# Performance work log

Hardware: AMD Instinct MI355X
Metric: run time of the kernel (lower is better)

Reference implementation:

```python
import jax, jax.numpy as jnp
import numpy as np

B, S, D, H, F = 2, 2048, 2048, 16, 8192
HD = D // H  # 128
EPS = 1e-5


def setup_inputs() -> dict:
    key = jax.random.key(0)
    ks = jax.random.split(key, 10)
    s = 0.02
    return {
        "x": jax.random.normal(ks[0], (B, S, D), dtype=jnp.float32),
        "rms_w": jnp.ones((D,), dtype=jnp.float32),
        "w_qkv": jax.random.normal(ks[1], (3 * D, D), dtype=jnp.float32) * s,
        "w_out": jax.random.normal(ks[2], (D, D), dtype=jnp.float32) * s,
        "w1": jax.random.normal(ks[3], (F, D), dtype=jnp.float32) * s,
        "b1": jnp.zeros((F,), dtype=jnp.float32),
        "w3": jax.random.normal(ks[4], (F, D), dtype=jnp.float32) * s,
        "b3": jnp.zeros((F,), dtype=jnp.float32),
        "w2": jax.random.normal(ks[5], (D, F), dtype=jnp.float32) * s,
        "b2": jnp.zeros((D,), dtype=jnp.float32),
    }


def reference(x, rms_w, w_qkv, w_out, w1, b1, w3, b3, w2, b2):
    b, s, d = x.shape
    # RMSNorm (computed in fp32 as in original)
    xf = x.astype(jnp.float32)
    xn = (xf * jax.lax.rsqrt(jnp.mean(xf * xf, axis=-1, keepdims=True) + EPS)).astype(x.dtype) * rms_w
    # QKV projection: Linear(dim, 3*dim, bias=False) then 'b n (qkv h d) -> qkv b h n d'
    qkv = jnp.einsum('bsd,ed->bse', xn, w_qkv).reshape(b, s, 3, H, HD)
    qkv = jnp.transpose(qkv, (2, 0, 3, 1, 4))  # [3, b, h, s, hd]
    q, k, v = qkv[0], qkv[1], qkv[2]
    # Naive causal attention with explicit [b,h,s,s] score matrix
    scores = jnp.einsum('bhqd,bhkd->bhqk', q, k) / jnp.sqrt(jnp.float32(HD)).astype(x.dtype)
    causal = jnp.tril(jnp.ones((s, s), dtype=bool))
    scores = jnp.where(causal[None, None], scores, -jnp.inf)
    p = jax.nn.softmax(scores, axis=-1)
    # dropout p=0.0 -> identity
    out = jnp.einsum('bhqk,bhkd->bhqd', p, v)
    # Faithful to original: .view(bs, seqlen, h*d) on [b,h,s,hd] = raw row-major reshape
    out = out.reshape(b, s, H * HD)
    h = out @ w_out.T
    # FeedForward: w2(w1(h) + relu(w3(h))), biases per nn.Linear defaults
    ffn = ((h @ w1.T + b1) + jax.nn.relu(h @ w3.T + b3)) @ w2.T + b2
    return x + ffn
```

## Files before the change

kernel.cpp:

```cpp
#include <hip/hip_runtime.h>
#include <hip/hip_bf16.h>
#include <cstdint>

#define BB 2
#define SS 2048
#define DD 2048
#define HH 16
#define HD 128
#define FF 8192
#define QKVD 6144

typedef __bf16 bf16x8 __attribute__((ext_vector_type(8)));
typedef float floatx4 __attribute__((ext_vector_type(4)));

#define LOG2E 1.4426950408889634f

__device__ __forceinline__ unsigned short f2bf(float f) {
  unsigned u = __builtin_bit_cast(unsigned, f);
  u += 0x7FFFu + ((u >> 16) & 1u);
  return (unsigned short)(u >> 16);
}
__device__ __forceinline__ float bf2f(unsigned short h) {
  return __builtin_bit_cast(float, (unsigned)h << 16);
}

__device__ __forceinline__ void load_lds_16B(const void* g, void* l) {
  __builtin_amdgcn_global_load_lds(
      (const __attribute__((address_space(1))) unsigned int*)g,
      (__attribute__((address_space(3))) unsigned int*)l, 16, 0, 0);
}

__global__ void f32_to_bf16_vec(const float* __restrict__ src,
                                unsigned short* __restrict__ dst, int n4) {
  int i = blockIdx.x * 256 + threadIdx.x;
  if (i < n4) {
    float4 v = ((const float4*)src)[i];
    ushort4 o;
    o.x = f2bf(v.x); o.y = f2bf(v.y); o.z = f2bf(v.z); o.w = f2bf(v.w);
    ((ushort4*)dst)[i] = o;
  }
}

__global__ __launch_bounds__(256) void rmsnorm_bf16(const float* __restrict__ x,
                                                    const float* __restrict__ w,
                                                    unsigned short* __restrict__ xn) {
  const int row = blockIdx.x, tid = threadIdx.x;
  const float4* xr = (const float4*)(x + (size_t)row * DD);
  float4 a = xr[tid], b = xr[tid + 256];
  float ss = a.x * a.x + a.y * a.y + a.z * a.z + a.w * a.w +
             b.x * b.x + b.y * b.y + b.z * b.z + b.w * b.w;
#pragma unroll
  for (int off = 1; off < 64; off <<= 1) ss += __shfl_xor(ss, off);
  __shared__ float red[4];
  if ((tid & 63) == 0) red[tid >> 6] = ss;
  __syncthreads();
  float tot = red[0] + red[1] + red[2] + red[3];
  float sc = rsqrtf(tot * (1.0f / (float)DD) + 1e-5f);
  const float4* wr = (const float4*)w;
  float4 wa = wr[tid], wb = wr[tid + 256];
  ushort4 oa, ob;
  oa.x = f2bf(a.x * sc * wa.x); oa.y = f2bf(a.y * sc * wa.y);
  oa.z = f2bf(a.z * sc * wa.z); oa.w = f2bf(a.w * sc * wa.w);
  ob.x = f2bf(b.x * sc * wb.x); ob.y = f2bf(b.y * sc * wb.y);
  ob.z = f2bf(b.z * sc * wb.z); ob.w = f2bf(b.w * sc * wb.w);
  *(ushort4*)&xn[(size_t)row * DD + tid * 4] = oa;
  *(ushort4*)&xn[(size_t)row * DD + (tid + 256) * 4] = ob;
}

template <int MODE>
__global__ __launch_bounds__(512, 1) void gemm_bt(
    const unsigned short* __restrict__ A, const unsigned short* __restrict__ Bw,
    void* __restrict__ Cout, const float* __restrict__ bias,
    const unsigned short* __restrict__ aux, const float* __restrict__ res,
    int M, int N, int K) {
  __shared__ __align__(16) unsigned short As[2][2][128 * 64];
  __shared__ __align__(16) unsigned short Bs[2][2][128 * 64];
  const int tid = threadIdx.x;
  const int lane = tid & 63, w = tid >> 6;
  const int l16 = lane & 15, quad = lane >> 4;
  const int wm = w >> 2, wn = w & 3;

  const int gx = gridDim.x;
  const int nwg = gx * gridDim.y;
  const int bid = blockIdx.y * gx + blockIdx.x;
  const int cpx = nwg >> 3;
  const int swzb = (bid & 7) * cpx + (bid >> 3);
  const int n0 = (swzb % gx) * 256, m0 = (swzb / gx) * 256;

  const int NT = K >> 6, NIT = NT >> 1;

  const int sr = lane >> 3, sc = lane & 7;
  const unsigned short* pA0 = A + (size_t)(m0 + w * 8 + sr) * K + (sc ^ sr) * 8;
  const unsigned short* pA1 = pA0 + (size_t)128 * K;
  const unsigned short* pB0 =
      Bw + (size_t)(n0 + (w >> 2) * 64 + (w & 3) * 8 + sr) * K + (sc ^ sr) * 8;
  const unsigned short* pB1 = pB0 + (size_t)128 * K;

#define STAGE_A(d, h, kt)                                              \
  {                                                                    \
    const int _k = ((kt) < NT ? (kt) : NT - 1) * 64;                   \
    const size_t _ho = (size_t)(h) * 64 * K;                           \
    load_lds_16B(pA0 + _ho + _k, &As[d][h][(w * 8) * 64]);             \
    load_lds_16B(pA1 + _ho + _k, &As[d][h][(64 + w * 8) * 64]);        \
  }
#define STAGE_B(d, h, kt)                                              \
  {                                                                    \
    const int _k = ((kt) < NT ? (kt) : NT - 1) * 64;                   \
    const size_t _ho = (size_t)(h) * 32 * K;                           \
    load_lds_16B(pB0 + _ho + _k, &Bs[d][h][(w * 8) * 64]);             \
    load_lds_16B(pB1 + _ho + _k, &Bs[d][h][(64 + w * 8) * 64]);        \
  }

  floatx4 acc[2][2][4][2];
#pragma unroll
  for (int a0 = 0; a0 < 2; a0++)
#pragma unroll
    for (int a1 = 0; a1 < 2; a1++)
#pragma unroll
      for (int a2 = 0; a2 < 4; a2++)
#pragma unroll
        for (int a3 = 0; a3 < 2; a3++) acc[a0][a1][a2][a3] = floatx4{0.f, 0.f, 0.f, 0.f};
  bf16x8 bb[2][2];

#define PHASE(d, mq, nq, LOADB, STAGES, VMW)                                    \
  {                                                                             \
    bf16x8 a_[4][2];                                                            \
    _Pragma("unroll") for (int fr = 0; fr < 4; ++fr) {                          \
      const int lr_ = wm * 64 + fr * 16 + l16;                                  \
      _Pragma("unroll") for (int kc = 0; kc < 2; ++kc)                          \
        a_[fr][kc] = *(const bf16x8*)&As[d][mq]                                 \
            [lr_ * 64 + (((kc * 4 + quad) ^ (l16 & 7)) * 8)];                   \
    }                                                                           \
    if (LOADB) {                                                                \
      _Pragma("unroll") for (int fn = 0; fn < 2; ++fn) {                        \
        const int lr_ = wn * 32 + fn * 16 + l16;                                \
        _Pragma("unroll") for (int kc = 0; kc < 2; ++kc)                        \
          bb[fn][kc] = *(const bf16x8*)&Bs[d][nq]                               \
              [lr_ * 64 + (((kc * 4 + quad) ^ (l16 & 7)) * 8)];                 \
      }                                                                         \
    }                                                                           \
    STAGES                                                                      \
    __builtin_amdgcn_s_barrier();                                               \
    asm volatile("s_waitcnt lgkmcnt(0)" ::: "memory");                          \
    __builtin_amdgcn_sched_barrier(0);                                          \
    __builtin_amdgcn_s_setprio(1);                                              \
    _Pragma("unroll") for (int kc = 0; kc < 2; ++kc)                            \
      _Pragma("unroll") for (int fr = 0; fr < 4; ++fr)                          \
        _Pragma("unroll") for (int fn = 0; fn < 2; ++fn)                        \
          acc[mq][nq][fr][fn] = __builtin_amdgcn_mfma_f32_16x16x32_bf16(        \
              a_[fr][kc], bb[fn][kc], acc[mq][nq][fr][fn], 0, 0, 0);            \
    __builtin_amdgcn_s_setprio(0);                                              \
    if (VMW) asm volatile("s_waitcnt vmcnt(4)" ::: "memory");                   \
    __builtin_amdgcn_s_barrier();                                               \
    asm volatile("" ::: "memory");                                              \
  }

  STAGE_A(0, 0, 0)
  STAGE_A(0, 1, 0)
  STAGE_B(0, 0, 0)
  STAGE_B(0, 1, 0)
  STAGE_B(1, 0, 1)
  STAGE_A(1, 0, 1)
  asm volatile("s_waitcnt vmcnt(4)" ::: "memory");
  __builtin_amdgcn_s_barrier();
  asm volatile("" ::: "memory");

#pragma unroll 1
  for (int it = 0; it < NIT; ++it) {
    const int t1 = 2 * it + 1, tn0 = 2 * it + 2, tn1 = 2 * it + 3;
    PHASE(0, 0, 0, true,  STAGE_A(1, 1, t1) STAGE_B(1, 1, t1), false)
    PHASE(0, 1, 0, false, , false)
    PHASE(0, 0, 1, true,  STAGE_B(0, 0, tn0), false)
    PHASE(0, 1, 1, false, STAGE_A(0, 0, tn0), true)
    PHASE(1, 0, 0, true,  STAGE_A(0, 1, tn0) STAGE_B(0, 1, tn0), false)
    PHASE(1, 1, 0, false, , false)
    PHASE(1, 0, 1, true,  STAGE_B(1, 0, tn1), false)
    PHASE(1, 1, 1, false, STAGE_A(1, 0, tn1), true)
  }
  asm volatile("s_waitcnt vmcnt(0)" ::: "memory");
#undef PHASE
#undef STAGE_A
#undef STAGE_B

#pragma unroll
  for (int nq = 0; nq < 2; ++nq)
#pragma unroll
    for (int fn = 0; fn < 2; ++fn) {
      const int col = n0 + wn * 64 + nq * 32 + fn * 16 + l16;
      float bv = 0.0f;
      if constexpr (MODE >= 1) bv = bias[col];
#pragma unroll
      for (int mq = 0; mq < 2; ++mq)
#pragma unroll
        for (int fr = 0; fr < 4; ++fr) {
          const int row0 = m0 + wm * 128 + mq * 64 + fr * 16 + quad * 4;
#pragma unroll
          for (int r = 0; r < 4; ++r) {
            const size_t idx = (size_t)(row0 + r) * N + col;
            float v = acc[mq][nq][fr][fn][r];
            if constexpr (MODE == 0) {
              ((unsigned short*)Cout)[idx] = f2bf(v);
            } else if constexpr (MODE == 1) {
              ((unsigned short*)Cout)[idx] = f2bf(v + bv);
            } else if constexpr (MODE == 2) {
              float t = fmaxf(v + bv, 0.0f) + bf2f(aux[idx]);
              ((unsigned short*)Cout)[idx] = f2bf(t);
            } else {
              ((float*)Cout)[idx] = v + bv + res[idx];
            }
          }
        }
    }
}

__global__ __launch_bounds__(256) void attn_fwd(const unsigned short* __restrict__ qkv,
                                                unsigned short* __restrict__ out) {
  __shared__ __align__(16) unsigned short Ks[64 * 136];
  __shared__ __align__(16) unsigned short Vt[128 * 72];
  __shared__ __align__(16) unsigned short Ps[4][32 * 72];
  const int tid = threadIdx.x;
  const int lane = tid & 63, wave = tid >> 6;
  const int l16 = lane & 15, quad = lane >> 4;
  const int p = blockIdx.x, h = blockIdx.y, b = blockIdx.z;
  const float scale = 0.088388347648318447f;

#pragma unroll 1
  for (int pass = 0; pass < 2; pass++) {
    const int qt = pass == 0 ? 15 - p : p;
    const int q0w = qt * 128 + wave * 32;
    const int ntiles = 2 * qt + 2;

    bf16x8 aq[2][4];
#pragma unroll
    for (int mi = 0; mi < 2; mi++) {
      const unsigned short* Qp =
          qkv + (size_t)(b * SS + q0w + mi * 16 + l16) * QKVD + h * HD + quad * 8;
#pragma unroll
      for (int kc = 0; kc < 4; kc++) aq[mi][kc] = *(const bf16x8*)(Qp + kc * 32);
    }

    floatx4 o[2][8];
    float m_r[2][4], l_r[2][4];
#pragma unroll
    for (int mi = 0; mi < 2; mi++) {
#pragma unroll
      for (int nb = 0; nb < 8; nb++) o[mi][nb] = floatx4{0.f, 0.f, 0.f, 0.f};
#pragma unroll
      for (int r = 0; r < 4; r++) { m_r[mi][r] = -1e30f; l_r[mi][r] = 0.f; }
    }

#pragma unroll 1
    for (int t = 0; t < ntiles; t++) {
      const int kv0 = t * 64;
      const bool need_mask = (t >= ntiles - 2);
      __syncthreads();
      {
        const int cc = tid & 15;
#pragma unroll
        for (int i = 0; i < 4; i++) {
          const int r = (tid >> 4) + 16 * i;
          const size_t rowb = (size_t)(b * SS + kv0 + r) * QKVD + h * HD + cc * 8;
          *(uint4*)&Ks[r * 136 + cc * 8] = *(const uint4*)(qkv + rowb + DD);
          unsigned short tmp[8];
          *(uint4*)tmp = *(const uint4*)(qkv + rowb + 2 * DD);
#pragma unroll
          for (int j2 = 0; j2 < 8; j2++) {
            const int d = cc * 8 + j2;
            Vt[d * 72 + (((r >> 3) + (d >> 3)) & 7) * 8 + (r & 7)] = tmp[j2];
          }
        }
      }
      __syncthreads();

      floatx4 s[2][4];
#pragma unroll
      for (int mi = 0; mi < 2; mi++)
#pragma unroll
        for (int ni = 0; ni < 4; ni++) s[mi][ni] = floatx4{0.f, 0.f, 0.f, 0.f};
#pragma unroll
      for (int kc = 0; kc < 4; kc++) {
        bf16x8 bk[4];
#pragma unroll
        for (int ni = 0; ni < 4; ni++)
          bk[ni] = *(const bf16x8*)&Ks[(ni * 16 + l16) * 136 + kc * 32 + quad * 8];
#pragma unroll
        for (int mi = 0; mi < 2; mi++)
#pragma unroll
          for (int ni = 0; ni < 4; ni++)
            s[mi][ni] = __builtin_amdgcn_mfma_f32_16x16x32_bf16(aq[mi][kc], bk[ni],
                                                                s[mi][ni], 0, 0, 0);
      }

#pragma unroll
      for (int mi = 0; mi < 2; mi++) {
        float alpha[4];
#pragma unroll
        for (int r = 0; r < 4; r++) {
          const int qrow = q0w + mi * 16 + quad * 4 + r;
          float v[4];
#pragma unroll
          for (int ni = 0; ni < 4; ni++) {
            v[ni] = s[mi][ni][r] * scale;
            if (need_mask && (kv0 + ni * 16 + l16 > qrow)) v[ni] = -1e30f;
          }
          float mx = fmaxf(fmaxf(v[0], v[1]), fmaxf(v[2], v[3]));
          mx = fmaxf(mx, __shfl_xor(mx, 1));
          mx = fmaxf(mx, __shfl_xor(mx, 2));
          mx = fmaxf(mx, __shfl_xor(mx, 4));
          mx = fmaxf(mx, __shfl_xor(mx, 8));
          const float mnew = fmaxf(m_r[mi][r], mx);
          alpha[r] = exp2f((m_r[mi][r] - mnew) * LOG2E);
          m_r[mi][r] = mnew;
          float rs = 0.f;
#pragma unroll
          for (int ni = 0; ni < 4; ni++) {
            v[ni] = exp2f((v[ni] - mnew) * LOG2E);
            rs += v[ni];
          }
          rs += __shfl_xor(rs, 1);
          rs += __shfl_xor(rs, 2);
          rs += __shfl_xor(rs, 4);
          rs += __shfl_xor(rs, 8);
          l_r[mi][r] = l_r[mi][r] * alpha[r] + rs;
          unsigned short* Pw = &Ps[wave][(mi * 16 + quad * 4 + r) * 72 + l16];
#pragma unroll
          for (int ni = 0; ni < 4; ni++) Pw[ni * 16] = f2bf(v[ni]);
        }
#pragma unroll
        for (int nb = 0; nb < 8; nb++)
#pragma unroll
          for (int r = 0; r < 4; r++) o[mi][nb][r] *= alpha[r];
      }
      asm volatile("s_waitcnt lgkmcnt(0)" ::: "memory");

      bf16x8 pa[2][2];
#pragma unroll
      for (int mi = 0; mi < 2; mi++)
#pragma unroll
        for (int kc2 = 0; kc2 < 2; kc2++)
          pa[mi][kc2] =
              *(const bf16x8*)&Ps[wave][(mi * 16 + l16) * 72 + kc2 * 32 + quad * 8];
#pragma unroll
      for (int nb = 0; nb < 8; nb++) {
        const int d = nb * 16 + l16;
#pragma unroll
        for (int kc2 = 0; kc2 < 2; kc2++) {
          const int chunk = kc2 * 4 + quad;
          bf16x8 bv = *(const bf16x8*)&Vt[d * 72 + ((chunk + (d >> 3)) & 7) * 8];
#pragma unroll
          for (int mi = 0; mi < 2; mi++)
            o[mi][nb] = __builtin_amdgcn_mfma_f32_16x16x32_bf16(pa[mi][kc2], bv,
                                                                o[mi][nb], 0, 0, 0);
        }
      }
    }

#pragma unroll
    for (int mi = 0; mi < 2; mi++) {
      unsigned short* Op =
          out + (size_t)((b * HH + h) * SS + q0w + mi * 16 + quad * 4) * HD + l16;
#pragma unroll
      for (int nb = 0; nb < 8; nb++)
#pragma unroll
        for (int r = 0; r < 4; r++)
          Op[(size_t)r * HD + nb * 16] = f2bf(o[mi][nb][r] / l_r[mi][r]);
    }
  }
}

extern "C" void kernel_launch(void* const* d_in, const int* in_sizes, int n_in,
                              void* d_out, int out_size, void* d_ws, size_t ws_size,
                              hipStream_t stream) {
  const float* x = (const float*)d_in[0];
  const float* rms_w = (const float*)d_in[1];
  const float* w_qkv = (const float*)d_in[2];
  const float* w_out = (const float*)d_in[3];
  const float* w1 = (const float*)d_in[4];
  const float* b1 = (const float*)d_in[5];
  const float* w3 = (const float*)d_in[6];
  const float* b3 = (const float*)d_in[7];
  const float* w2 = (const float*)d_in[8];
  const float* b2 = (const float*)d_in[9];
  float* out = (float*)d_out;

  char* ws = (char*)d_ws;
  size_t off = 0;
  auto alloc = [&](size_t bytes) {
    char* p = ws + off;
    off += (bytes + 255) & ~(size_t)255;
    return p;
  };
  const int M = BB * SS;
  unsigned short* wqkv_b = (unsigned short*)alloc((size_t)QKVD * DD * 2);
  unsigned short* wout_b = (unsigned short*)alloc((size_t)DD * DD * 2);
  unsigned short* w1_b = (unsigned short*)alloc((size_t)FF * DD * 2);
  unsigned short* w3_b = (unsigned short*)alloc((size_t)FF * DD * 2);
  unsigned short* w2_b = (unsigned short*)alloc((size_t)DD * FF * 2);
  unsigned short* xn_b = (unsigned short*)alloc((size_t)M * DD * 2);
  unsigned short* qkv_b = (unsigned short*)alloc((size_t)M * QKVD * 2);
  unsigned short* attn_b = (unsigned short*)alloc((size_t)M * DD * 2);
  unsigned short* h_b = (unsigned short*)alloc((size_t)M * DD * 2);
  unsigned short* act_b = (unsigned short*)alloc((size_t)M * FF * 2);

  f32_to_bf16_vec<<<(QKVD * DD / 4) / 256, 256, 0, stream>>>(w_qkv, wqkv_b, QKVD * DD / 4);
  f32_to_bf16_vec<<<(DD * DD / 4) / 256, 256, 0, stream>>>(w_out, wout_b, DD * DD / 4);
  f32_to_bf16_vec<<<(FF * DD / 4) / 256, 256, 0, stream>>>(w1, w1_b, FF * DD / 4);
  f32_to_bf16_vec<<<(FF * DD / 4) / 256, 256, 0, stream>>>(w3, w3_b, FF * DD / 4);
  f32_to_bf16_vec<<<(DD * FF / 4) / 256, 256, 0, stream>>>(w2, w2_b, DD * FF / 4);

  rmsnorm_bf16<<<M, 256, 0, stream>>>(x, rms_w, xn_b);

  gemm_bt<0><<<dim3(QKVD / 256, M / 256), 512, 0, stream>>>(
      xn_b, wqkv_b, qkv_b, nullptr, nullptr, nullptr, M, QKVD, DD);

  attn_fwd<<<dim3(8, HH, BB), 256, 0, stream>>>(qkv_b, attn_b);

  gemm_bt<0><<<dim3(DD / 256, M / 256), 512, 0, stream>>>(
      attn_b, wout_b, h_b, nullptr, nullptr, nullptr, M, DD, DD);

  gemm_bt<1><<<dim3(FF / 256, M / 256), 512, 0, stream>>>(
      h_b, w1_b, act_b, b1, nullptr, nullptr, M, FF, DD);

  gemm_bt<2><<<dim3(FF / 256, M / 256), 512, 0, stream>>>(
      h_b, w3_b, act_b, b3, act_b, nullptr, M, FF, DD);

  gemm_bt<3><<<dim3(DD / 256, M / 256), 512, 0, stream>>>(
      act_b, w2_b, out, b2, nullptr, x, M, DD, FF);
}
```

Baseline: 1.302 ms.

## Split-K the out-projection and w2 GEMMs with separate reduction kernels

The two GEMMs with N=2048 (attention out-projection and the FFN down-projection) now split K in two across blockIdx.z. Each half writes fp32 partials into reused workspace, and new reduce kernels sum them, applying the bias, residual and bf16 conversion. This doubles the block count from 128 so that more CUs are occupied. In exchange it adds extra fp32 partial writes and reads plus two small kernel launches.

```diff
diff --git a/kernel.cpp b/kernel.cpp
--- a/kernel.cpp
+++ b/kernel.cpp
@@ -67,12 +67,45 @@
   *(ushort4*)&xn[(size_t)row * DD + (tid + 256) * 4] = ob;
 }
 
+__global__ __launch_bounds__(256) void reduce_wout(const float* __restrict__ p,
+                                                   unsigned short* __restrict__ outb,
+                                                   int n4) {
+  int i = blockIdx.x * 256 + threadIdx.x;
+  if (i < n4) {
+    float4 a = ((const float4*)p)[i];
+    float4 b = ((const float4*)(p + (size_t)BB * SS * DD))[i];
+    ushort4 o;
+    o.x = f2bf(a.x + b.x); o.y = f2bf(a.y + b.y);
+    o.z = f2bf(a.z + b.z); o.w = f2bf(a.w + b.w);
+    ((ushort4*)outb)[i] = o;
+  }
+}
+
+__global__ __launch_bounds__(256) void reduce_w2(const float* __restrict__ p,
+                                                 const float* __restrict__ b2,
+                                                 const float* __restrict__ x,
+                                                 float* __restrict__ out, int n4) {
+  int i = blockIdx.x * 256 + threadIdx.x;
+  if (i < n4) {
+    float4 a = ((const float4*)p)[i];
+    float4 b = ((const float4*)(p + (size_t)BB * SS * DD))[i];
+    float4 xx = ((const float4*)x)[i];
+    float4 bb = ((const float4*)b2)[i & (DD / 4 - 1)];
+    float4 o;
+    o.x = a.x + b.x + bb.x + xx.x;
+    o.y = a.y + b.y + bb.y + xx.y;
+    o.z = a.z + b.z + bb.z + xx.z;
+    o.w = a.w + b.w + bb.w + xx.w;
+    ((float4*)out)[i] = o;
+  }
+}
+
 template <int MODE>
 __global__ __launch_bounds__(512, 1) void gemm_bt(
     const unsigned short* __restrict__ A, const unsigned short* __restrict__ Bw,
     void* __restrict__ Cout, const float* __restrict__ bias,
     const unsigned short* __restrict__ aux, const float* __restrict__ res,
-    int M, int N, int K) {
+    int M, int N, int K, int lda) {
   __shared__ __align__(16) unsigned short As[2][2][128 * 64];
   __shared__ __align__(16) unsigned short Bs[2][2][128 * 64];
   const int tid = threadIdx.x;
@@ -86,27 +119,29 @@
   const int cpx = nwg >> 3;
   const int swzb = (bid & 7) * cpx + (bid >> 3);
   const int n0 = (swzb % gx) * 256, m0 = (swzb / gx) * 256;
+  const size_t koff = (size_t)blockIdx.z * K;
 
   const int NT = K >> 6, NIT = NT >> 1;
 
   const int sr = lane >> 3, sc = lane & 7;
-  const unsigned short* pA0 = A + (size_t)(m0 + w * 8 + sr) * K + (sc ^ sr) * 8;
-  const unsigned short* pA1 = pA0 + (size_t)128 * K;
+  const unsigned short* pA0 =
+      A + (size_t)(m0 + w * 8 + sr) * lda + koff + (sc ^ sr) * 8;
+  const unsigned short* pA1 = pA0 + (size_t)128 * lda;
   const unsigned short* pB0 =
-      Bw + (size_t)(n0 + (w >> 2) * 64 + (w & 3) * 8 + sr) * K + (sc ^ sr) * 8;
-  const unsigned short* pB1 = pB0 + (size_t)128 * K;
+      Bw + (size_t)(n0 + (w >> 2) * 64 + (w & 3) * 8 + sr) * lda + koff + (sc ^ sr) * 8;
+  const unsigned short* pB1 = pB0 + (size_t)128 * lda;
 
 #define STAGE_A(d, h, kt)                                              \
   {                                                                    \
     const int _k = ((kt) < NT ? (kt) : NT - 1) * 64;                   \
-    const size_t _ho = (size_t)(h) * 64 * K;                           \
+    const size_t _ho = (size_t)(h) * 64 * lda;                         \
     load_lds_16B(pA0 + _ho + _k, &As[d][h][(w * 8) * 64]);             \
     load_lds_16B(pA1 + _ho + _k, &As[d][h][(64 + w * 8) * 64]);        \
   }
 #define STAGE_B(d, h, kt)                                              \
   {                                                                    \
     const int _k = ((kt) < NT ? (kt) : NT - 1) * 64;                   \
-    const size_t _ho = (size_t)(h) * 32 * K;                           \
+    const size_t _ho = (size_t)(h) * 32 * lda;                         \
     load_lds_16B(pB0 + _ho + _k, &Bs[d][h][(w * 8) * 64]);             \
     load_lds_16B(pB1 + _ho + _k, &Bs[d][h][(64 + w * 8) * 64]);        \
   }
@@ -188,7 +223,7 @@
     for (int fn = 0; fn < 2; ++fn) {
       const int col = n0 + wn * 64 + nq * 32 + fn * 16 + l16;
       float bv = 0.0f;
-      if constexpr (MODE >= 1) bv = bias[col];
+      if constexpr (MODE >= 1 && MODE <= 3) bv = bias[col];
 #pragma unroll
       for (int mq = 0; mq < 2; ++mq)
 #pragma unroll
@@ -205,8 +240,10 @@
             } else if constexpr (MODE == 2) {
               float t = fmaxf(v + bv, 0.0f) + bf2f(aux[idx]);
               ((unsigned short*)Cout)[idx] = f2bf(t);
+            } else if constexpr (MODE == 3) {
+              ((float*)Cout)[idx] = v + bv + res[idx];
             } else {
-              ((float*)Cout)[idx] = v + bv + res[idx];
+              ((float*)Cout)[(size_t)blockIdx.z * ((size_t)M * N) + idx] = v;
             }
           }
         }
@@ -401,6 +438,7 @@
   unsigned short* attn_b = (unsigned short*)alloc((size_t)M * DD * 2);
   unsigned short* h_b = (unsigned short*)alloc((size_t)M * DD * 2);
   unsigned short* act_b = (unsigned short*)alloc((size_t)M * FF * 2);
+  float* part = (float*)xn_b;
 
   f32_to_bf16_vec<<<(QKVD * DD / 4) / 256, 256, 0, stream>>>(w_qkv, wqkv_b, QKVD * DD / 4);
   f32_to_bf16_vec<<<(DD * DD / 4) / 256, 256, 0, stream>>>(w_out, wout_b, DD * DD / 4);
@@ -411,19 +449,21 @@
   rmsnorm_bf16<<<M, 256, 0, stream>>>(x, rms_w, xn_b);
 
   gemm_bt<0><<<dim3(QKVD / 256, M / 256), 512, 0, stream>>>(
-      xn_b, wqkv_b, qkv_b, nullptr, nullptr, nullptr, M, QKVD, DD);
+      xn_b, wqkv_b, qkv_b, nullptr, nullptr, nullptr, M, QKVD, DD, DD);
 
   attn_fwd<<<dim3(8, HH, BB), 256, 0, stream>>>(qkv_b, attn_b);
 
-  gemm_bt<0><<<dim3(DD / 256, M / 256), 512, 0, stream>>>(
-      attn_b, wout_b, h_b, nullptr, nullptr, nullptr, M, DD, DD);
+  gemm_bt<4><<<dim3(DD / 256, M / 256, 2), 512, 0, stream>>>(
+      attn_b, wout_b, part, nullptr, nullptr, nullptr, M, DD, DD / 2, DD);
+  reduce_wout<<<(M * DD / 4) / 256, 256, 0, stream>>>(part, h_b, M * DD / 4);
 
   gemm_bt<1><<<dim3(FF / 256, M / 256), 512, 0, stream>>>(
-      h_b, w1_b, act_b, b1, nullptr, nullptr, M, FF, DD);
+      h_b, w1_b, act_b, b1, nullptr, nullptr, M, FF, DD, DD);
 
   gemm_bt<2><<<dim3(FF / 256, M / 256), 512, 0, stream>>>(
-      h_b, w3_b, act_b, b3, act_b, nullptr, M, FF, DD);
-
-  gemm_bt<3><<<dim3(DD / 256, M / 256), 512, 0, stream>>>(
-      act_b, w2_b, out, b2, nullptr, x, M, DD, FF);
-}
+      h_b, w3_b, act_b, b3, act_b, nullptr, M, FF, DD, DD);
+
+  gemm_bt<4><<<dim3(DD / 256, M / 256, 2), 512, 0, stream>>>(
+      act_b, w2_b, part, nullptr, nullptr, nullptr, M, DD, FF / 2, FF);
+  reduce_w2<<<(M * DD / 4) / 256, 256, 0, stream>>>(part, b2, x, out, M * DD / 4);
+}
```

Measured after the change: 1.189 ms. 1.09x faster.
